# Optimization experiments

Measured on AMD Instinct MI355X. Metric: run time of the kernel, lower is better.

The kernel has to match this reference:

```python
import jax, jax.numpy as jnp
import numpy as np

MARGIN = 0.0


def setup_inputs() -> dict:
    key = jax.random.key(0)
    k1, k2, k3 = jax.random.split(key, 3)
    n, d = 8192, 128
    inputs = jax.random.normal(k1, (n, d), dtype=jnp.float32)
    targets = jax.random.randint(k2, (n,), 0, 512, dtype=jnp.int64)
    cids = jax.random.randint(k3, (n,), 0, 8, dtype=jnp.int64)
    return {"inputs": inputs, "targets": targets, "cids": cids}


def _margin_ranking_loss(x1, x2, margin):
    # nn.MarginRankingLoss with y=1: mean(max(0, -(x1 - x2) + margin))
    return jnp.mean(jnp.maximum(x2 - x1 + margin, 0.0))


def reference(inputs, targets, cids):
    n = inputs.shape[0]
    # pairwise euclidean distance matrix [n, n]
    sq = jnp.sum(inputs * inputs, axis=1)              # [n]
    d2 = sq[:, None] + sq[None, :] - 2.0 * (inputs @ inputs.T)
    dist = jnp.sqrt(jnp.clip(d2, 1e-12, 1e12))         # [n, n]

    mask = targets[:, None] == targets[None, :]        # [n, n] same-identity
    # view_mask (cids) is computed in the original but never used

    # hardest positive (max over same-id, incl. self) and hardest negative (min over diff-id)
    pos_masked = jnp.where(mask, dist, -jnp.inf)
    neg_masked = jnp.where(mask, jnp.inf, dist)
    dist_ap = jnp.max(pos_masked, axis=1)              # [n]
    dist_an = jnp.min(neg_masked, axis=1)              # [n]
    p2_ind = jnp.argmax(pos_masked, axis=1)            # [n]
    n1_ind = jnp.argmin(neg_masked, axis=1)            # [n]

    # secondary neighbors: hardest-negative of the hardest negative,
    # hardest-positive of the hardest positive (row lookups)
    dist_n12 = dist_an[n1_ind]                         # min of dist[n1_ind] over ~mask[n1_ind]
    dist_p12 = dist_ap[p2_ind]                         # max of dist[p2_ind] over mask[p2_ind]

    loss = (_margin_ranking_loss(dist_an, dist_ap, MARGIN)
            + 0.1 * _margin_ranking_loss(dist_n12, dist_ap, MARGIN)
            + 0.1 * _margin_ranking_loss(dist_an, dist_p12, MARGIN))
    prec = jnp.mean((dist_an > dist_ap).astype(jnp.float32))
    return loss, prec, dist
```

## Files before the change

kernel.cpp:

```cpp
#include <hip/hip_runtime.h>

#define NROWS 8192
#define DDIM 128

typedef unsigned short u16;
typedef unsigned int u32;
typedef unsigned long long u64;
typedef __attribute__((ext_vector_type(4))) float f32x4;
typedef __attribute__((ext_vector_type(4), aligned(8))) float f32x4u;
typedef __attribute__((ext_vector_type(2))) float f32x2;
typedef __attribute__((ext_vector_type(4))) int i32x4;
typedef __attribute__((ext_vector_type(8))) short short8;

__device__ __forceinline__ u16 f32_to_bf16(float f){
  u32 u = __float_as_uint(f);
  u32 r = (u + 0x7FFFu + ((u >> 16) & 1u)) >> 16;
  return (u16)r;
}
__device__ __forceinline__ float bf16_to_f32(u16 h){ return __uint_as_float(((u32)h) << 16); }

__global__ __launch_bounds__(256) void pack_kernel(const float* __restrict__ in,
                                                   u16* __restrict__ phi, u16* __restrict__ plo,
                                                   float* __restrict__ sq,
                                                   u64* __restrict__ pos_key, u64* __restrict__ neg_key){
  int t = blockIdx.x * 256 + threadIdx.x;
  if (t < NROWS){ pos_key[t] = 0ull; neg_key[t] = 0xFFFFFFFFFFFFFFFFull; }
  int r = t >> 4, s = t & 15;
  const float* src = in + (size_t)r * DDIM + s * 8;
  f32x4 a = *(const f32x4*)(src);
  f32x4 b = *(const f32x4*)(src + 4);
  float x[8] = {a.x, a.y, a.z, a.w, b.x, b.y, b.z, b.w};
  short8 hv, lv;
  float ss = 0.f;
  #pragma unroll
  for (int j = 0; j < 8; ++j){
    u16 h = f32_to_bf16(x[j]);
    u16 l = f32_to_bf16(x[j] - bf16_to_f32(h));
    hv[j] = (short)h; lv[j] = (short)l;
    ss += x[j] * x[j];
  }
  size_t dst = (((size_t)(r >> 4) * 4 + (s >> 2)) * 64 + (s & 3) * 16 + (r & 15)) * 8;
  *(short8*)(phi + dst) = hv;
  *(short8*)(plo + dst) = lv;
  #pragma unroll
  for (int m = 1; m < 16; m <<= 1) ss += __shfl_xor(ss, m, 64);
  if (s == 0) sq[r] = ss;
}

__global__ __launch_bounds__(256, 3) void dist_kernel(
    const u16* __restrict__ phi, const u16* __restrict__ plo,
    const float* __restrict__ sq, const int* __restrict__ tgt,
    float* __restrict__ dist, u64* __restrict__ pos_key, u64* __restrict__ neg_key)
{
  int id = blockIdx.x;
  int xcd = id & 7, r9 = id >> 3;
  int cx = xcd >> 1, cy = xcd & 1;
  const int bi = cx * 16 + (r9 >> 5);
  const int bj = cy * 32 + (r9 & 31);

  const int tid = threadIdx.x;
  const int w = tid >> 6, lane = tid & 63;
  const int wr = w >> 1, wc = w & 1;
  const int lr = lane & 15, g = lane >> 4;

  f32x4 acc[4][4] = {};

  short8 bufA[2][8], bufB[2][8];
  #pragma unroll
  for (int m = 0; m < 4; ++m){
    size_t offA = ((size_t)(((bi * 8 + wr * 4 + m) * 4 + 0) * 64) + lane) * 8;
    bufA[0][m * 2 + 0] = *(const short8*)(phi + offA);
    bufA[0][m * 2 + 1] = *(const short8*)(plo + offA);
    size_t offB = ((size_t)(((bj * 8 + wc * 4 + m) * 4 + 0) * 64) + lane) * 8;
    bufB[0][m * 2 + 0] = *(const short8*)(phi + offB);
    bufB[0][m * 2 + 1] = *(const short8*)(plo + offB);
  }
  #pragma unroll
  for (int kk = 0; kk < 4; ++kk){
    const int cur = kk & 1, nxt = cur ^ 1;
    if (kk < 3){
      #pragma unroll
      for (int m = 0; m < 4; ++m){
        size_t offA = ((size_t)(((bi * 8 + wr * 4 + m) * 4 + (kk + 1)) * 64) + lane) * 8;
        bufA[nxt][m * 2 + 0] = *(const short8*)(phi + offA);
        bufA[nxt][m * 2 + 1] = *(const short8*)(plo + offA);
        size_t offB = ((size_t)(((bj * 8 + wc * 4 + m) * 4 + (kk + 1)) * 64) + lane) * 8;
        bufB[nxt][m * 2 + 0] = *(const short8*)(phi + offB);
        bufB[nxt][m * 2 + 1] = *(const short8*)(plo + offB);
      }
    }
    #pragma unroll
    for (int m = 0; m < 4; ++m)
      #pragma unroll
      for (int n = 0; n < 4; ++n){
        acc[m][n] = __builtin_amdgcn_mfma_f32_16x16x32_bf16(bufB[cur][n*2+0], bufA[cur][m*2+0], acc[m][n], 0, 0, 0);
        acc[m][n] = __builtin_amdgcn_mfma_f32_16x16x32_bf16(bufB[cur][n*2+1], bufA[cur][m*2+0], acc[m][n], 0, 0, 0);
        acc[m][n] = __builtin_amdgcn_mfma_f32_16x16x32_bf16(bufB[cur][n*2+0], bufA[cur][m*2+1], acc[m][n], 0, 0, 0);
      }
  }

  f32x4 sqc[4]; i32x4 tcv[4]; int cbase[4];
  #pragma unroll
  for (int n = 0; n < 4; ++n){
    cbase[n] = bj * 128 + wc * 64 + n * 16 + g * 4;
    sqc[n] = *(const f32x4*)(sq + cbase[n]);
    tcv[n] = *(const i32x4*)(tgt + cbase[n]);
  }
  #pragma unroll
  for (int m = 0; m < 4; ++m){
    const int grow = bi * 128 + wr * 64 + m * 16 + lr;
    const float sqr = sq[grow];
    const int tr = tgt[grow];
    float bpv = -1.f, bnv = 3.0e38f; int bpc = 0x7FFFFFFF, bnc = 0x7FFFFFFF;
    float* drow = dist + (size_t)grow * NROWS;
    #pragma unroll
    for (int n = 0; n < 4; ++n){
      f32x4 dd4;
      #pragma unroll
      for (int r = 0; r < 4; ++r){
        float d2 = sqr + sqc[n][r] - 2.f * acc[m][n][r];
        d2 = fmaxf(d2, 1e-12f);
        dd4[r] = __builtin_amdgcn_sqrtf(d2);
        if (tr == tcv[n][r]){
          if (d2 > bpv){ bpv = d2; bpc = cbase[n] + r; }
        } else {
          if (d2 < bnv){ bnv = d2; bnc = cbase[n] + r; }
        }
      }
      *(f32x4u*)(drow + cbase[n]) = dd4;
    }
    #pragma unroll
    for (int msk = 16; msk <= 32; msk <<= 1){
      float ov = __shfl_xor(bpv, msk, 64); int oc = __shfl_xor(bpc, msk, 64);
      if (ov > bpv || (ov == bpv && oc < bpc)){ bpv = ov; bpc = oc; }
      ov = __shfl_xor(bnv, msk, 64); oc = __shfl_xor(bnc, msk, 64);
      if (ov < bnv || (ov == bnv && oc < bnc)){ bnv = ov; bnc = oc; }
    }
    if (g == 0){
      if (bpv >= 0.f)
        atomicMax(&pos_key[grow],
                  ((u64)__float_as_uint(__builtin_amdgcn_sqrtf(bpv)) << 32) | (u64)(0xFFFFFFFFu - (u32)bpc));
      if (bnv < 3.0e38f)
        atomicMin(&neg_key[grow],
                  ((u64)__float_as_uint(__builtin_amdgcn_sqrtf(bnv)) << 32) | (u64)(u32)bnc);
    }
  }
}

__global__ __launch_bounds__(1024) void final_kernel(const u64* __restrict__ pk, const u64* __restrict__ nk,
                                                     float* __restrict__ out){
  __shared__ float s_ap[NROWS];
  __shared__ float s_an[NROWS];
  int tid = threadIdx.x;
  int p2r[8], n1r[8];
  #pragma unroll
  for (int j = 0; j < 8; ++j){
    int i = tid + j * 1024;
    u64 p = pk[i], q = nk[i];
    s_ap[i] = __uint_as_float((u32)(p >> 32));
    s_an[i] = __uint_as_float((u32)(q >> 32));
    p2r[j] = (int)(0xFFFFFFFFu - (u32)(p & 0xFFFFFFFFu));
    n1r[j] = (int)(u32)(q & 0xFFFFFFFFu);
  }
  __syncthreads();
  float s1 = 0.f, s2 = 0.f, s3 = 0.f; float pc = 0.f;
  #pragma unroll
  for (int j = 0; j < 8; ++j){
    int i = tid + j * 1024;
    float a = s_ap[i], b = s_an[i];
    float n12 = s_an[n1r[j]];
    float p12 = s_ap[p2r[j]];
    s1 += fmaxf(a - b, 0.f);
    s2 += fmaxf(a - n12, 0.f);
    s3 += fmaxf(p12 - b, 0.f);
    pc += (b > a) ? 1.f : 0.f;
  }
  __syncthreads();
  float* r1 = s_ap; float* r2 = s_ap + 1024; float* r3 = s_an; float* r4 = s_an + 1024;
  r1[tid] = s1; r2[tid] = s2; r3[tid] = s3; r4[tid] = pc;
  __syncthreads();
  for (int s = 512; s > 0; s >>= 1){
    if (tid < s){ r1[tid] += r1[tid + s]; r2[tid] += r2[tid + s]; r3[tid] += r3[tid + s]; r4[tid] += r4[tid + s]; }
    __syncthreads();
  }
  if (tid == 0){
    float inv = 1.f / (float)NROWS;
    out[0] = r1[0] * inv + 0.1f * (r2[0] * inv) + 0.1f * (r3[0] * inv);
    out[1] = r4[0] * inv;
  }
}

extern "C" void kernel_launch(void* const* d_in, const int* in_sizes, int n_in,
                              void* d_out, int out_size, void* d_ws, size_t ws_size,
                              hipStream_t stream){
  const float* inputs = (const float*)d_in[0];
  const int* targets = (const int*)d_in[1];
  float* out = (float*)d_out;
  char* ws = (char*)d_ws;

  u16* phi = (u16*)ws;
  u16* plo = (u16*)(ws + (2u << 20));
  float* sq = (float*)(ws + (4u << 20));
  u64* pos_key = (u64*)(ws + (4u << 20) + (64u << 10));
  u64* neg_key = (u64*)(ws + (4u << 20) + (128u << 10));

  pack_kernel<<<(NROWS * 16) / 256, 256, 0, stream>>>(inputs, phi, plo, sq, pos_key, neg_key);
  dist_kernel<<<64 * 64, 256, 0, stream>>>(phi, plo, sq, targets, out + 2, pos_key, neg_key);
  final_kernel<<<1, 1024, 0, stream>>>(pos_key, neg_key, out);
}
```

Baseline: 127.3 us.

## Retile distance kernel to row strips streaming column tiles with register-resident rows

Each block now handles 16 rows against a 2048-column quarter, keeping the row fragments in registers and streaming column fragments with double buffering across 8 steps. The hardest-positive/negative reduction is accumulated per row across all steps, so each block issues fewer atomics. This aims at better store locality and less atomic contention, at the cost of lower operand reuse (more column-fragment loads per MFMA) and smaller per-wave tiles.

```diff
diff --git a/kernel.cpp b/kernel.cpp
--- a/kernel.cpp
+++ b/kernel.cpp
@@ -53,97 +53,97 @@
     float* __restrict__ dist, u64* __restrict__ pos_key, u64* __restrict__ neg_key)
 {
   int id = blockIdx.x;
-  int xcd = id & 7, r9 = id >> 3;
-  int cx = xcd >> 1, cy = xcd & 1;
-  const int bi = cx * 16 + (r9 >> 5);
-  const int bj = cy * 32 + (r9 & 31);
+  int xcd = id & 7, r8 = id >> 3;
+  const int rg = xcd * 64 + (r8 >> 2);
+  const int q  = r8 & 3;
 
   const int tid = threadIdx.x;
   const int w = tid >> 6, lane = tid & 63;
-  const int wr = w >> 1, wc = w & 1;
   const int lr = lane & 15, g = lane >> 4;
 
-  f32x4 acc[4][4] = {};
-
-  short8 bufA[2][8], bufB[2][8];
-  #pragma unroll
-  for (int m = 0; m < 4; ++m){
-    size_t offA = ((size_t)(((bi * 8 + wr * 4 + m) * 4 + 0) * 64) + lane) * 8;
-    bufA[0][m * 2 + 0] = *(const short8*)(phi + offA);
-    bufA[0][m * 2 + 1] = *(const short8*)(plo + offA);
-    size_t offB = ((size_t)(((bj * 8 + wc * 4 + m) * 4 + 0) * 64) + lane) * 8;
-    bufB[0][m * 2 + 0] = *(const short8*)(phi + offB);
-    bufB[0][m * 2 + 1] = *(const short8*)(plo + offB);
-  }
+  const int row  = rg * 16 + lr;
+  const int colw = q * 2048 + w * 512;
+
+  short8 ahi[4], alo[4];
   #pragma unroll
   for (int kk = 0; kk < 4; ++kk){
-    const int cur = kk & 1, nxt = cur ^ 1;
-    if (kk < 3){
+    size_t offA = ((size_t)((rg * 4 + kk) * 64) + lane) * 8;
+    ahi[kk] = *(const short8*)(phi + offA);
+    alo[kk] = *(const short8*)(plo + offA);
+  }
+  const float sqr = sq[row];
+  const int   tr  = tgt[row];
+  float* drow = dist + (size_t)row * NROWS;
+
+  float bpv = -1.f, bnv = 3.0e38f; int bpc = 0x7FFFFFFF, bnc = 0x7FFFFFFF;
+
+  short8 bhi[2][4], blo[2][4];
+  const int p00 = q * 128 + w * 32;
+
+  #define LOADB(p, S, KK)                                              \
+    _Pragma("unroll")                                                  \
+    for (int n_ = 0; n_ < 4; ++n_){                                    \
+      size_t off = ((size_t)(((p00 + (S) * 4 + n_) * 4 + (KK)) * 64) + lane) * 8; \
+      bhi[p][n_] = *(const short8*)(phi + off);                        \
+      blo[p][n_] = *(const short8*)(plo + off);                        \
+    }
+
+  LOADB(0, 0, 0);
+
+  for (int s = 0; s < 8; ++s){
+    f32x4 acc[4] = {};
+    #pragma unroll
+    for (int kk = 0; kk < 4; ++kk){
+      const int cur = kk & 1, nxt = cur ^ 1;
+      if (kk < 3){
+        LOADB(nxt, s, kk + 1);
+      } else if (s < 7){
+        LOADB(nxt, s + 1, 0);
+      }
       #pragma unroll
-      for (int m = 0; m < 4; ++m){
-        size_t offA = ((size_t)(((bi * 8 + wr * 4 + m) * 4 + (kk + 1)) * 64) + lane) * 8;
-        bufA[nxt][m * 2 + 0] = *(const short8*)(phi + offA);
-        bufA[nxt][m * 2 + 1] = *(const short8*)(plo + offA);
-        size_t offB = ((size_t)(((bj * 8 + wc * 4 + m) * 4 + (kk + 1)) * 64) + lane) * 8;
-        bufB[nxt][m * 2 + 0] = *(const short8*)(phi + offB);
-        bufB[nxt][m * 2 + 1] = *(const short8*)(plo + offB);
+      for (int n = 0; n < 4; ++n){
+        acc[n] = __builtin_amdgcn_mfma_f32_16x16x32_bf16(bhi[cur][n], ahi[kk], acc[n], 0, 0, 0);
+        acc[n] = __builtin_amdgcn_mfma_f32_16x16x32_bf16(blo[cur][n], ahi[kk], acc[n], 0, 0, 0);
+        acc[n] = __builtin_amdgcn_mfma_f32_16x16x32_bf16(bhi[cur][n], alo[kk], acc[n], 0, 0, 0);
       }
     }
-    #pragma unroll
-    for (int m = 0; m < 4; ++m)
-      #pragma unroll
-      for (int n = 0; n < 4; ++n){
-        acc[m][n] = __builtin_amdgcn_mfma_f32_16x16x32_bf16(bufB[cur][n*2+0], bufA[cur][m*2+0], acc[m][n], 0, 0, 0);
-        acc[m][n] = __builtin_amdgcn_mfma_f32_16x16x32_bf16(bufB[cur][n*2+1], bufA[cur][m*2+0], acc[m][n], 0, 0, 0);
-        acc[m][n] = __builtin_amdgcn_mfma_f32_16x16x32_bf16(bufB[cur][n*2+0], bufA[cur][m*2+1], acc[m][n], 0, 0, 0);
-      }
-  }
-
-  f32x4 sqc[4]; i32x4 tcv[4]; int cbase[4];
-  #pragma unroll
-  for (int n = 0; n < 4; ++n){
-    cbase[n] = bj * 128 + wc * 64 + n * 16 + g * 4;
-    sqc[n] = *(const f32x4*)(sq + cbase[n]);
-    tcv[n] = *(const i32x4*)(tgt + cbase[n]);
-  }
-  #pragma unroll
-  for (int m = 0; m < 4; ++m){
-    const int grow = bi * 128 + wr * 64 + m * 16 + lr;
-    const float sqr = sq[grow];
-    const int tr = tgt[grow];
-    float bpv = -1.f, bnv = 3.0e38f; int bpc = 0x7FFFFFFF, bnc = 0x7FFFFFFF;
-    float* drow = dist + (size_t)grow * NROWS;
+    const int cb0 = colw + s * 64;
     #pragma unroll
     for (int n = 0; n < 4; ++n){
+      const int cb = cb0 + n * 16 + g * 4;
+      f32x4 sqc = *(const f32x4*)(sq + cb);
+      i32x4 tcv = *(const i32x4*)(tgt + cb);
       f32x4 dd4;
       #pragma unroll
       for (int r = 0; r < 4; ++r){
-        float d2 = sqr + sqc[n][r] - 2.f * acc[m][n][r];
+        float d2 = sqr + sqc[r] - 2.f * acc[n][r];
         d2 = fmaxf(d2, 1e-12f);
         dd4[r] = __builtin_amdgcn_sqrtf(d2);
-        if (tr == tcv[n][r]){
-          if (d2 > bpv){ bpv = d2; bpc = cbase[n] + r; }
+        if (tr == tcv[r]){
+          if (d2 > bpv){ bpv = d2; bpc = cb + r; }
         } else {
-          if (d2 < bnv){ bnv = d2; bnc = cbase[n] + r; }
+          if (d2 < bnv){ bnv = d2; bnc = cb + r; }
         }
       }
-      *(f32x4u*)(drow + cbase[n]) = dd4;
+      *(f32x4u*)(drow + cb) = dd4;
     }
-    #pragma unroll
-    for (int msk = 16; msk <= 32; msk <<= 1){
-      float ov = __shfl_xor(bpv, msk, 64); int oc = __shfl_xor(bpc, msk, 64);
-      if (ov > bpv || (ov == bpv && oc < bpc)){ bpv = ov; bpc = oc; }
-      ov = __shfl_xor(bnv, msk, 64); oc = __shfl_xor(bnc, msk, 64);
-      if (ov < bnv || (ov == bnv && oc < bnc)){ bnv = ov; bnc = oc; }
-    }
-    if (g == 0){
-      if (bpv >= 0.f)
-        atomicMax(&pos_key[grow],
-                  ((u64)__float_as_uint(__builtin_amdgcn_sqrtf(bpv)) << 32) | (u64)(0xFFFFFFFFu - (u32)bpc));
-      if (bnv < 3.0e38f)
-        atomicMin(&neg_key[grow],
-                  ((u64)__float_as_uint(__builtin_amdgcn_sqrtf(bnv)) << 32) | (u64)(u32)bnc);
-    }
+  }
+  #undef LOADB
+
+  #pragma unroll
+  for (int msk = 16; msk <= 32; msk <<= 1){
+    float ov = __shfl_xor(bpv, msk, 64); int oc = __shfl_xor(bpc, msk, 64);
+    if (ov > bpv || (ov == bpv && oc < bpc)){ bpv = ov; bpc = oc; }
+    ov = __shfl_xor(bnv, msk, 64); oc = __shfl_xor(bnc, msk, 64);
+    if (ov < bnv || (ov == bnv && oc < bnc)){ bnv = ov; bnc = oc; }
+  }
+  if (g == 0){
+    if (bpv >= 0.f)
+      atomicMax(&pos_key[row],
+                ((u64)__float_as_uint(__builtin_amdgcn_sqrtf(bpv)) << 32) | (u64)(0xFFFFFFFFu - (u32)bpc));
+    if (bnv < 3.0e38f)
+      atomicMin(&neg_key[row],
+                ((u64)__float_as_uint(__builtin_amdgcn_sqrtf(bnv)) << 32) | (u64)(u32)bnc);
   }
 }
 
@@ -205,6 +205,6 @@
   u64* neg_key = (u64*)(ws + (4u << 20) + (128u << 10));
 
   pack_kernel<<<(NROWS * 16) / 256, 256, 0, stream>>>(inputs, phi, plo, sq, pos_key, neg_key);
-  dist_kernel<<<64 * 64, 256, 0, stream>>>(phi, plo, sq, targets, out + 2, pos_key, neg_key);
+  dist_kernel<<<2048, 256, 0, stream>>>(phi, plo, sq, targets, out + 2, pos_key, neg_key);
   final_kernel<<<1, 1024, 0, stream>>>(pos_key, neg_key, out);
 }
```

Result: slower. 145.5 us (+14.3%).
